# Performance work log

Measured on AMD Instinct MI355X. Metric: run time of the kernel, lower is better.

The kernel has to match this reference:

```python
import jax, jax.numpy as jnp
import numpy as np

N_NODES = 100000
N_EDGES = 1600000
IN_DIM = 256
HEADS = 4
OUT_DIM = 32
NEG_SLOPE = 0.2


def setup_inputs() -> dict:
    key = jax.random.key(0)
    ks = jax.random.split(key, 6)
    x = jax.random.normal(ks[0], (N_NODES, IN_DIM), dtype=jnp.float32)
    # xavier-ish init scale for fc and attention vectors
    W = jax.random.normal(ks[1], (IN_DIM, HEADS * OUT_DIM), dtype=jnp.float32) * (1.0 / np.sqrt(IN_DIM))
    attn_l = jax.random.normal(ks[2], (HEADS, OUT_DIM), dtype=jnp.float32) * (1.0 / np.sqrt(OUT_DIM))
    attn_r = jax.random.normal(ks[3], (HEADS, OUT_DIM), dtype=jnp.float32) * (1.0 / np.sqrt(OUT_DIM))
    src = jax.random.randint(ks[4], (N_EDGES,), 0, N_NODES, dtype=jnp.int32)
    dst = jax.random.randint(ks[5], (N_EDGES,), 0, N_NODES, dtype=jnp.int32)
    return {"x": x, "W": W, "attn_l": attn_l, "attn_r": attn_r, "src": src, "dst": dst}


def reference(x, W, attn_l, attn_r, src, dst):
    N = x.shape[0]
    H, D = attn_l.shape
    # shared linear projection (feat_drop = 0)
    feat = (x @ W).reshape(N, H, D)                      # [N,H,D]
    el = jnp.sum(feat * attn_l, axis=-1)                 # [N,H]
    er = jnp.sum(feat * attn_r, axis=-1)                 # [N,H]
    e = jax.nn.leaky_relu(el[src] + er[dst], NEG_SLOPE)  # [E,H]
    # edge softmax over incoming edges of each destination node
    m = jax.ops.segment_max(e, dst, num_segments=N)      # [N,H]
    m = jnp.where(jnp.isfinite(m), m, 0.0)               # zero-in-degree guard
    ex = jnp.exp(e - m[dst])                             # [E,H]
    denom = jax.ops.segment_sum(ex, dst, num_segments=N) # [N,H]
    a = ex / jnp.maximum(denom[dst], 1e-9)               # [E,H] (attn_drop = 0)
    # weighted scatter-add aggregation
    out = jax.ops.segment_sum(a[:, :, None] * feat[src], dst, num_segments=N)  # [N,H,D]
    # head mean (the .mean(1) in GAT1.forward)
    return out.mean(axis=1)                              # [N,D]
```

## Files before the change

kernel.cpp:

```cpp
#include <hip/hip_runtime.h>
#include <math.h>

#define NN 100000
#define NE 1600000
#define IN_DIM 256
#define HD 128
#define NEG_SLOPE 0.2f

#define B1SH 9
#define NPB (1 << B1SH)
#define NB1 ((NN + NPB - 1) / NPB)
#define SC_BLOCKS ((NE / 4 + 1023) / 1024)

typedef __attribute__((ext_vector_type(8))) __bf16 bf16x8;
typedef __attribute__((ext_vector_type(4))) float floatx4;

__device__ inline unsigned short f2bf(float f) {
    unsigned int b = __float_as_uint(f);
    b += 0x7fffu + ((b >> 16) & 1u);
    return (unsigned short)(b >> 16);
}
__device__ inline unsigned int pk(float lo, float hi) {
    return (unsigned int)f2bf(lo) | ((unsigned int)f2bf(hi) << 16);
}
__device__ inline float bflo(unsigned int u) { return __uint_as_float(u << 16); }
__device__ inline float bfhi(unsigned int u) { return __uint_as_float(u & 0xffff0000u); }
__device__ inline float lrelu(float v) { return (v > 0.f) ? v : v * NEG_SLOPE; }

__global__ __launch_bounds__(256) void prep_w_kernel(const float* __restrict__ W,
                                                     unsigned int* __restrict__ wswz) {
    int g = blockIdx.x * 256 + threadIdx.x;
    int lane = g & 63;
    int t = (g >> 6) & 7;
    int c = g >> 9;
    int sub = lane & 15, quad = lane >> 4;
    int n = t * 16 + sub;
    int kbase = c * 32 + quad * 8;
    unsigned int ob = (unsigned int)g * 4;
#pragma unroll
    for (int i = 0; i < 4; ++i) {
        float lo = W[(size_t)(kbase + 2 * i) * HD + n];
        float hi = W[(size_t)(kbase + 2 * i + 1) * HD + n];
        wswz[ob + i] = pk(lo, hi);
    }
}

__global__ __launch_bounds__(256) void gemm_kernel(const float* __restrict__ x,
                                                   const uint4* __restrict__ wswz,
                                                   const float* __restrict__ attn_l,
                                                   const float* __restrict__ attn_r,
                                                   unsigned short* __restrict__ featb,
                                                   float* __restrict__ el,
                                                   float* __restrict__ er) {
    const int tid = threadIdx.x;
    const int lane = tid & 63, wv = tid >> 6;
    const int sub = lane & 15, quad = lane >> 4;
    const int row0 = blockIdx.x * 64 + wv * 16;

    int m = row0 + sub;
    if (m >= NN) m = NN - 1;
    const float* xp = x + (size_t)m * IN_DIM + quad * 8;

    bf16x8 af[8];
#pragma unroll
    for (int h = 0; h < 2; ++h) {
        float4 raw[4][2];
#pragma unroll
        for (int c = 0; c < 4; ++c) {
            raw[c][0] = *(const float4*)(xp + (h * 4 + c) * 32);
            raw[c][1] = *(const float4*)(xp + (h * 4 + c) * 32 + 4);
        }
#pragma unroll
        for (int c = 0; c < 4; ++c) {
            uint4 au;
            au.x = pk(raw[c][0].x, raw[c][0].y);
            au.y = pk(raw[c][0].z, raw[c][0].w);
            au.z = pk(raw[c][1].x, raw[c][1].y);
            au.w = pk(raw[c][1].z, raw[c][1].w);
            af[h * 4 + c] = __builtin_bit_cast(bf16x8, au);
        }
    }

    floatx4 acc[8];
#pragma unroll
    for (int t = 0; t < 8; ++t) acc[t] = (floatx4){0.f, 0.f, 0.f, 0.f};

#pragma unroll
    for (int c = 0; c < 8; ++c) {
        uint4 bu[8];
#pragma unroll
        for (int t = 0; t < 8; ++t) bu[t] = wswz[(c * 8 + t) * 64 + lane];
#pragma unroll
        for (int t = 0; t < 8; ++t) {
            bf16x8 bfr = __builtin_bit_cast(bf16x8, bu[t]);
            acc[t] = __builtin_amdgcn_mfma_f32_16x16x32_bf16(af[c], bfr, acc[t], 0, 0, 0);
        }
    }

    float al[8], ar[8];
#pragma unroll
    for (int t = 0; t < 8; ++t) {
        al[t] = attn_l[t * 16 + sub];
        ar[t] = attn_r[t * 16 + sub];
    }

#pragma unroll
    for (int r = 0; r < 4; ++r) {
        int row = row0 + quad * 4 + r;
        uint4 fv;
        fv.x = pk(acc[0][r], acc[1][r]);
        fv.y = pk(acc[2][r], acc[3][r]);
        fv.z = pk(acc[4][r], acc[5][r]);
        fv.w = pk(acc[6][r], acc[7][r]);
        float pl[4], pr[4];
#pragma unroll
        for (int hh = 0; hh < 4; ++hh) {
            pl[hh] = acc[2 * hh][r] * al[2 * hh] + acc[2 * hh + 1][r] * al[2 * hh + 1];
            pr[hh] = acc[2 * hh][r] * ar[2 * hh] + acc[2 * hh + 1][r] * ar[2 * hh + 1];
        }
#pragma unroll
        for (int o = 1; o < 16; o <<= 1) {
#pragma unroll
            for (int hh = 0; hh < 4; ++hh) {
                pl[hh] += __shfl_xor(pl[hh], o);
                pr[hh] += __shfl_xor(pr[hh], o);
            }
        }
        if (row < NN) {
            *(uint4*)(featb + (size_t)row * HD + sub * 8) = fv;
            if (sub < 4) {
                float vl = (sub == 0) ? pl[0] : (sub == 1) ? pl[1] : (sub == 2) ? pl[2] : pl[3];
                float vr = (sub == 0) ? pr[0] : (sub == 1) ? pr[1] : (sub == 2) ? pr[2] : pr[3];
                el[row * 4 + sub] = vl;
                er[row * 4 + sub] = vr;
            }
        }
    }
}

__global__ __launch_bounds__(256) void precount_kernel(const int4* __restrict__ dst4,
                                                       int* __restrict__ gbcnt) {
    __shared__ int cnt[NB1];
    int t = threadIdx.x;
    for (int i = t; i < NB1; i += 256) cnt[i] = 0;
    __syncthreads();
    int base4 = blockIdx.x * 1024;
#pragma unroll
    for (int k = 0; k < 4; ++k) {
        int gi = base4 + k * 256 + t;
        if (gi < NE / 4) {
            int4 d = dst4[gi];
            atomicAdd(&cnt[d.x >> B1SH], 1);
            atomicAdd(&cnt[d.y >> B1SH], 1);
            atomicAdd(&cnt[d.z >> B1SH], 1);
            atomicAdd(&cnt[d.w >> B1SH], 1);
        }
    }
    __syncthreads();
    for (int i = t; i < NB1; i += 256)
        if (cnt[i]) atomicAdd(&gbcnt[i], cnt[i]);
}

__global__ __launch_bounds__(256) void bscan_kernel(const int* __restrict__ gbcnt,
                                                    int* __restrict__ regstart,
                                                    int* __restrict__ gcursor,
                                                    int* __restrict__ offs) {
    __shared__ int sh[256];
    int t = threadIdx.x;
    int v = (t < NB1) ? gbcnt[t] : 0;
    sh[t] = v;
    __syncthreads();
    for (int o = 1; o < 256; o <<= 1) {
        int a = (t >= o) ? sh[t - o] : 0;
        __syncthreads();
        sh[t] += a;
        __syncthreads();
    }
    int excl = sh[t] - v;
    if (t < NB1) {
        regstart[t] = excl;
        gcursor[t] = excl;
    }
    if (t == 0) {
        regstart[NB1] = NE;
        offs[NN] = NE;
    }
}

__global__ __launch_bounds__(256) void scatter_kernel(const int4* __restrict__ src4,
                                                      const int4* __restrict__ dst4,
                                                      int* __restrict__ gcursor,
                                                      unsigned int* __restrict__ pkd) {
    __shared__ int cnt[NB1];
    __shared__ int gbase[NB1];
    int t = threadIdx.x;
    for (int i = t; i < NB1; i += 256) cnt[i] = 0;
    __syncthreads();

    int base4 = blockIdx.x * 1024;
    unsigned int pkv[16];
    unsigned int brk[16];
#pragma unroll
    for (int k = 0; k < 4; ++k) {
        int gi = base4 + k * 256 + t;
        bool ok = gi < NE / 4;
        int gic = ok ? gi : 0;
        int4 s = src4[gic];
        int4 d = dst4[gic];
        int dd[4] = {d.x, d.y, d.z, d.w};
        int ss[4] = {s.x, s.y, s.z, s.w};
#pragma unroll
        for (int j4 = 0; j4 < 4; ++j4) {
            int e = k * 4 + j4;
            if (ok) {
                int b = dd[j4] >> B1SH;
                int r = atomicAdd(&cnt[b], 1);
                brk[e] = ((unsigned int)b << 12) | (unsigned int)r;
                pkv[e] = ((unsigned int)(dd[j4] & (NPB - 1)) << 17) | (unsigned int)ss[j4];
            } else {
                brk[e] = 0xFFFFFFFFu;
            }
        }
    }
    __syncthreads();
    for (int i = t; i < NB1; i += 256)
        gbase[i] = cnt[i] ? atomicAdd(&gcursor[i], cnt[i]) : 0;
    __syncthreads();
#pragma unroll
    for (int e = 0; e < 16; ++e) {
        if (brk[e] != 0xFFFFFFFFu) {
            int b = brk[e] >> 12;
            int r = brk[e] & 0xFFF;
            pkd[gbase[b] + r] = pkv[e];
        }
    }
}

__global__ __launch_bounds__(256) void build_kernel(const unsigned int* __restrict__ pkd,
                                                    const int* __restrict__ regstart,
                                                    int* __restrict__ offs,
                                                    int* __restrict__ csr_src) {
    __shared__ int fcnt[NPB];
    __shared__ int foffs[NPB];
    __shared__ int ssc[256];
    int b = blockIdx.x, t = threadIdx.x;
    int rs = regstart[b], re = regstart[b + 1];
    int n = re - rs;

    for (int i = t; i < NPB; i += 256) fcnt[i] = 0;
    __syncthreads();
    for (int i = t; i < n; i += 256) {
        unsigned int v = pkd[rs + i];
        atomicAdd(&fcnt[v >> 17], 1);
    }
    __syncthreads();
    int a0 = fcnt[2 * t], a1 = fcnt[2 * t + 1];
    int s = a0 + a1;
    ssc[t] = s;
    __syncthreads();
    for (int o = 1; o < 256; o <<= 1) {
        int u = (t >= o) ? ssc[t - o] : 0;
        __syncthreads();
        ssc[t] += u;
        __syncthreads();
    }
    int excl = ssc[t] - s;
    foffs[2 * t] = excl;
    foffs[2 * t + 1] = excl + a0;
    __syncthreads();
#pragma unroll
    for (int q = 0; q < 2; ++q) {
        int j = t + q * 256;
        int node = b * NPB + j;
        if (node < NN) offs[node] = rs + foffs[j];
    }
    for (int i = t; i < NPB; i += 256) fcnt[i] = 0;
    __syncthreads();
    int i = t;
    for (; i + 768 < n; i += 1024) {
        unsigned int v0 = pkd[rs + i];
        unsigned int v1 = pkd[rs + i + 256];
        unsigned int v2 = pkd[rs + i + 512];
        unsigned int v3 = pkd[rs + i + 768];
        int j0 = v0 >> 17, j1 = v1 >> 17, j2 = v2 >> 17, j3 = v3 >> 17;
        int r0 = atomicAdd(&fcnt[j0], 1);
        int r1 = atomicAdd(&fcnt[j1], 1);
        int r2 = atomicAdd(&fcnt[j2], 1);
        int r3 = atomicAdd(&fcnt[j3], 1);
        csr_src[rs + foffs[j0] + r0] = (int)(v0 & 0x1FFFFu);
        csr_src[rs + foffs[j1] + r1] = (int)(v1 & 0x1FFFFu);
        csr_src[rs + foffs[j2] + r2] = (int)(v2 & 0x1FFFFu);
        csr_src[rs + foffs[j3] + r3] = (int)(v3 & 0x1FFFFu);
    }
    for (; i < n; i += 256) {
        unsigned int v = pkd[rs + i];
        int j = v >> 17;
        int r = atomicAdd(&fcnt[j], 1);
        csr_src[rs + foffs[j] + r] = (int)(v & 0x1FFFFu);
    }
}

#define CH 32
__global__ __launch_bounds__(256) void aggregate_kernel(const uint4* __restrict__ featu4,
                                                        const float4* __restrict__ el4,
                                                        const float4* __restrict__ er4,
                                                        const int* __restrict__ offs,
                                                        const int* __restrict__ csr_src,
                                                        float* __restrict__ out) {
    __shared__ int    s_sv[4][4][CH + 1];
    __shared__ float4 s_a4[4][4][CH + 1];
    __shared__ int sdeg[16], smap[16];

    const int tid = threadIdx.x;
    const int lane = tid & 63, wv = tid >> 6;
    const int g = lane >> 4, sub = lane & 15;

    if (tid < 16) {
        int n0 = blockIdx.x * 16 + tid;
        sdeg[tid] = offs[n0 + 1] - offs[n0];
    }
    __syncthreads();
    if (tid < 16) {
        int d = sdeg[tid];
        int rank = 0;
#pragma unroll
        for (int j = 0; j < 16; ++j) {
            int dj = sdeg[j];
            rank += (dj < d) || (dj == d && j < tid);
        }
        smap[rank] = blockIdx.x * 16 + tid;
    }
    __syncthreads();
    const int node = smap[wv * 4 + g];
    const int beg = offs[node], end = offs[node + 1];

    const float4 erv = er4[node];
    float4 sm = make_float4(0.f, 0.f, 0.f, 0.f);
    float acc[8];
#pragma unroll
    for (int i = 0; i < 8; ++i) acc[i] = 0.f;

    for (int c0 = beg; c0 < end; c0 += CH) {
        int cnt = end - c0;
        if (cnt > CH) cnt = CH;
#pragma unroll
        for (int t = 0; t < 2; ++t) {
            int slot = sub + t * 16;
            int sv = 0;
            float4 w = make_float4(0.f, 0.f, 0.f, 0.f);
            if (slot < cnt) {
                sv = csr_src[c0 + slot];
                float4 e = el4[sv];
                w.x = __expf(lrelu(e.x + erv.x));
                w.y = __expf(lrelu(e.y + erv.y));
                w.z = __expf(lrelu(e.z + erv.z));
                w.w = __expf(lrelu(e.w + erv.w));
                sm.x += w.x; sm.y += w.y; sm.z += w.z; sm.w += w.w;
            }
            s_sv[wv][g][slot] = sv;
            s_a4[wv][g][slot] = w;
        }
        int rounds = (cnt + 7) >> 3;
        for (int jr = 0; jr < rounds; ++jr) {
            int jb = jr << 3;
            int sv[8];
#pragma unroll
            for (int e = 0; e < 8; ++e) sv[e] = s_sv[wv][g][jb + e];
            uint4 u[8];
#pragma unroll
            for (int e = 0; e < 8; ++e) u[e] = featu4[(size_t)sv[e] * 16 + sub];
            float4 w[8];
#pragma unroll
            for (int e = 0; e < 8; ++e) w[e] = s_a4[wv][g][jb + e];
#pragma unroll
            for (int e = 0; e < 8; ++e) {
                acc[0] = fmaf(w[e].x, bflo(u[e].x), acc[0]);
                acc[1] = fmaf(w[e].x, bfhi(u[e].x), acc[1]);
                acc[2] = fmaf(w[e].y, bflo(u[e].y), acc[2]);
                acc[3] = fmaf(w[e].y, bfhi(u[e].y), acc[3]);
                acc[4] = fmaf(w[e].z, bflo(u[e].z), acc[4]);
                acc[5] = fmaf(w[e].z, bfhi(u[e].z), acc[5]);
                acc[6] = fmaf(w[e].w, bflo(u[e].w), acc[6]);
                acc[7] = fmaf(w[e].w, bfhi(u[e].w), acc[7]);
            }
        }
    }

#pragma unroll
    for (int o = 1; o < 16; o <<= 1) {
        sm.x += __shfl_xor(sm.x, o);
        sm.y += __shfl_xor(sm.y, o);
        sm.z += __shfl_xor(sm.z, o);
        sm.w += __shfl_xor(sm.w, o);
    }
    float ix = 1.f / fmaxf(sm.x, 1e-9f);
    float iy = 1.f / fmaxf(sm.y, 1e-9f);
    float iz = 1.f / fmaxf(sm.z, 1e-9f);
    float iw = 1.f / fmaxf(sm.w, 1e-9f);
    float ox = 0.25f * (acc[0] * ix + acc[2] * iy + acc[4] * iz + acc[6] * iw);
    float oy = 0.25f * (acc[1] * ix + acc[3] * iy + acc[5] * iz + acc[7] * iw);
    out[node * 32 + sub]      = ox;
    out[node * 32 + 16 + sub] = oy;
}

extern "C" void kernel_launch(void* const* d_in, const int* in_sizes, int n_in,
                              void* d_out, int out_size, void* d_ws, size_t ws_size,
                              hipStream_t stream) {
    const float* x      = (const float*)d_in[0];
    const float* W      = (const float*)d_in[1];
    const float* attn_l = (const float*)d_in[2];
    const float* attn_r = (const float*)d_in[3];
    const int*   src    = (const int*)d_in[4];
    const int*   dst    = (const int*)d_in[5];
    float* out = (float*)d_out;

    char* p = (char*)d_ws;
    auto alloc = [&](size_t bytes) -> void* {
        void* r = (void*)p;
        p += (bytes + 255) & ~(size_t)255;
        return r;
    };
    unsigned short* featb = (unsigned short*)alloc((size_t)NN * HD * 2);
    unsigned int*   wswz  = (unsigned int*)alloc(4096 * 16);
    float* el      = (float*)alloc((size_t)NN * 4 * 4);
    float* er      = (float*)alloc((size_t)NN * 4 * 4);
    int*   offs    = (int*)alloc((size_t)(NN + 1) * 4);
    unsigned int* pkd = (unsigned int*)alloc((size_t)NE * 4);
    int*   csr     = (int*)alloc((size_t)NE * 4);
    int*   gbcnt   = (int*)alloc((size_t)NB1 * 4);
    int*   regstart= (int*)alloc((size_t)(NB1 + 1) * 4);
    int*   gcursor = (int*)alloc((size_t)NB1 * 4);

    hipMemsetAsync(gbcnt, 0, (size_t)NB1 * 4, stream);

    prep_w_kernel<<<16, 256, 0, stream>>>(W, wswz);
    gemm_kernel<<<(NN + 63) / 64, 256, 0, stream>>>(x, (const uint4*)wswz, attn_l, attn_r,
                                                    featb, el, er);
    precount_kernel<<<SC_BLOCKS, 256, 0, stream>>>((const int4*)dst, gbcnt);
    bscan_kernel<<<1, 256, 0, stream>>>(gbcnt, regstart, gcursor, offs);
    scatter_kernel<<<SC_BLOCKS, 256, 0, stream>>>((const int4*)src, (const int4*)dst,
                                                  gcursor, pkd);
    build_kernel<<<NB1, 256, 0, stream>>>(pkd, regstart, offs, csr);
    aggregate_kernel<<<NN / 16, 256, 0, stream>>>((const uint4*)featb, (const float4*)el,
                                                  (const float4*)er, offs, csr, out);
}
```

Measured before the change: 302.1 us.

## Double-buffer feature gathers in aggregation and use packed FMA accumulators

The aggregation loop is restructured so the gather of the first round of neighbour feature rows starts before the attention weights are computed. Each later round's gathers are issued before the FMAs of the current round, using two alternating register buffers. Accumulation switches to two-wide float vectors so the compiler can emit packed FMA instructions, and the launch bounds now request four blocks per SM. The extra buffered uint4 registers raise register pressure, and the occupancy hint may force spilling.

New measurement: 301.5 us. No clear change (-0.2%).

```diff
diff --git a/kernel.cpp b/kernel.cpp
--- a/kernel.cpp
+++ b/kernel.cpp
@@ -14,6 +14,7 @@
 
 typedef __attribute__((ext_vector_type(8))) __bf16 bf16x8;
 typedef __attribute__((ext_vector_type(4))) float floatx4;
+typedef __attribute__((ext_vector_type(2))) float f32x2;
 
 __device__ inline unsigned short f2bf(float f) {
     unsigned int b = __float_as_uint(f);
@@ -23,9 +24,13 @@
 __device__ inline unsigned int pk(float lo, float hi) {
     return (unsigned int)f2bf(lo) | ((unsigned int)f2bf(hi) << 16);
 }
-__device__ inline float bflo(unsigned int u) { return __uint_as_float(u << 16); }
-__device__ inline float bfhi(unsigned int u) { return __uint_as_float(u & 0xffff0000u); }
 __device__ inline float lrelu(float v) { return (v > 0.f) ? v : v * NEG_SLOPE; }
+__device__ inline f32x2 un2(unsigned int v) {
+    f32x2 r;
+    r.x = __uint_as_float(v << 16);
+    r.y = __uint_as_float(v & 0xffff0000u);
+    return r;
+}
 
 __global__ __launch_bounds__(256) void prep_w_kernel(const float* __restrict__ W,
                                                      unsigned int* __restrict__ wswz) {
@@ -301,12 +306,12 @@
 }
 
 #define CH 32
-__global__ __launch_bounds__(256) void aggregate_kernel(const uint4* __restrict__ featu4,
-                                                        const float4* __restrict__ el4,
-                                                        const float4* __restrict__ er4,
-                                                        const int* __restrict__ offs,
-                                                        const int* __restrict__ csr_src,
-                                                        float* __restrict__ out) {
+__global__ __launch_bounds__(256, 4) void aggregate_kernel(const uint4* __restrict__ featu4,
+                                                           const float4* __restrict__ el4,
+                                                           const float4* __restrict__ er4,
+                                                           const int* __restrict__ offs,
+                                                           const int* __restrict__ csr_src,
+                                                           float* __restrict__ out) {
     __shared__ int    s_sv[4][4][CH + 1];
     __shared__ float4 s_a4[4][4][CH + 1];
     __shared__ int sdeg[16], smap[16];
@@ -336,53 +341,92 @@
 
     const float4 erv = er4[node];
     float4 sm = make_float4(0.f, 0.f, 0.f, 0.f);
-    float acc[8];
-#pragma unroll
-    for (int i = 0; i < 8; ++i) acc[i] = 0.f;
+    f32x2 acc2[4];
+#pragma unroll
+    for (int i = 0; i < 4; ++i) acc2[i] = (f32x2){0.f, 0.f};
 
     for (int c0 = beg; c0 < end; c0 += CH) {
         int cnt = end - c0;
         if (cnt > CH) cnt = CH;
+
+        int svr[2];
 #pragma unroll
         for (int t = 0; t < 2; ++t) {
             int slot = sub + t * 16;
-            int sv = 0;
+            int sv = (slot < cnt) ? csr_src[c0 + slot] : 0;
+            svr[t] = sv;
+            s_sv[wv][g][slot] = sv * 16;
+        }
+
+        uint4 ua[8], ub[8];
+#pragma unroll
+        for (int e = 0; e < 8; ++e)
+            ua[e] = featu4[(size_t)s_sv[wv][g][e] + sub];
+
+#pragma unroll
+        for (int t = 0; t < 2; ++t) {
+            int slot = sub + t * 16;
             float4 w = make_float4(0.f, 0.f, 0.f, 0.f);
             if (slot < cnt) {
-                sv = csr_src[c0 + slot];
-                float4 e = el4[sv];
+                float4 e = el4[svr[t]];
                 w.x = __expf(lrelu(e.x + erv.x));
                 w.y = __expf(lrelu(e.y + erv.y));
                 w.z = __expf(lrelu(e.z + erv.z));
                 w.w = __expf(lrelu(e.w + erv.w));
                 sm.x += w.x; sm.y += w.y; sm.z += w.z; sm.w += w.w;
             }
-            s_sv[wv][g][slot] = sv;
             s_a4[wv][g][slot] = w;
         }
+
         int rounds = (cnt + 7) >> 3;
-        for (int jr = 0; jr < rounds; ++jr) {
-            int jb = jr << 3;
-            int sv[8];
-#pragma unroll
-            for (int e = 0; e < 8; ++e) sv[e] = s_sv[wv][g][jb + e];
-            uint4 u[8];
-#pragma unroll
-            for (int e = 0; e < 8; ++e) u[e] = featu4[(size_t)sv[e] * 16 + sub];
-            float4 w[8];
-#pragma unroll
-            for (int e = 0; e < 8; ++e) w[e] = s_a4[wv][g][jb + e];
-#pragma unroll
-            for (int e = 0; e < 8; ++e) {
-                acc[0] = fmaf(w[e].x, bflo(u[e].x), acc[0]);
-                acc[1] = fmaf(w[e].x, bfhi(u[e].x), acc[1]);
-                acc[2] = fmaf(w[e].y, bflo(u[e].y), acc[2]);
-                acc[3] = fmaf(w[e].y, bfhi(u[e].y), acc[3]);
-                acc[4] = fmaf(w[e].z, bflo(u[e].z), acc[4]);
-                acc[5] = fmaf(w[e].z, bfhi(u[e].z), acc[5]);
-                acc[6] = fmaf(w[e].w, bflo(u[e].w), acc[6]);
-                acc[7] = fmaf(w[e].w, bfhi(u[e].w), acc[7]);
-            }
+        int jr = 0;
+        while (true) {
+            bool m1 = (jr + 1) < rounds;
+            if (m1) {
+                int nb = (jr + 1) << 3;
+#pragma unroll
+                for (int e = 0; e < 8; ++e)
+                    ub[e] = featu4[(size_t)s_sv[wv][g][nb + e] + sub];
+            }
+            {
+                int jb = jr << 3;
+#pragma unroll
+                for (int e = 0; e < 8; ++e) {
+                    float4 we = s_a4[wv][g][jb + e];
+                    uint4 u = ua[e];
+                    f32x2 w0 = {we.x, we.x}, w1 = {we.y, we.y};
+                    f32x2 w2 = {we.z, we.z}, w3 = {we.w, we.w};
+                    acc2[0] = __builtin_elementwise_fma(w0, un2(u.x), acc2[0]);
+                    acc2[1] = __builtin_elementwise_fma(w1, un2(u.y), acc2[1]);
+                    acc2[2] = __builtin_elementwise_fma(w2, un2(u.z), acc2[2]);
+                    acc2[3] = __builtin_elementwise_fma(w3, un2(u.w), acc2[3]);
+                }
+            }
+            ++jr;
+            if (!m1) break;
+            bool m2 = (jr + 1) < rounds;
+            if (m2) {
+                int nb = (jr + 1) << 3;
+#pragma unroll
+                for (int e = 0; e < 8; ++e)
+                    ua[e] = featu4[(size_t)s_sv[wv][g][nb + e] + sub];
+            }
+            {
+                int jb = jr << 3;
+#pragma unroll
+                for (int e = 0; e < 8; ++e) {
+                    float4 we = s_a4[wv][g][jb + e];
+                    uint4 u = ub[e];
+                    f32x2 w0 = {we.x, we.x}, w1 = {we.y, we.y};
+                    f32x2 w2 = {we.z, we.z}, w3 = {we.w, we.w};
+                    acc2[0] = __builtin_elementwise_fma(w0, un2(u.x), acc2[0]);
+                    acc2[1] = __builtin_elementwise_fma(w1, un2(u.y), acc2[1]);
+                    acc2[2] = __builtin_elementwise_fma(w2, un2(u.z), acc2[2]);
+                    acc2[3] = __builtin_elementwise_fma(w3, un2(u.w), acc2[3]);
+                }
+            }
+            ++jr;
+            if (!m2) break;
         }
     }
 
@@ -397,8 +441,8 @@
     float iy = 1.f / fmaxf(sm.y, 1e-9f);
     float iz = 1.f / fmaxf(sm.z, 1e-9f);
     float iw = 1.f / fmaxf(sm.w, 1e-9f);
-    float ox = 0.25f * (acc[0] * ix + acc[2] * iy + acc[4] * iz + acc[6] * iw);
-    float oy = 0.25f * (acc[1] * ix + acc[3] * iy + acc[5] * iz + acc[7] * iw);
+    float ox = 0.25f * (acc2[0].x * ix + acc2[1].x * iy + acc2[2].x * iz + acc2[3].x * iw);
+    float oy = 0.25f * (acc2[0].y * ix + acc2[1].y * iy + acc2[2].y * iz + acc2[3].y * iw);
     out[node * 32 + sub]      = ox;
     out[node * 32 + 16 + sub] = oy;
 }
```
